# Optimization experiments

Measured on AMD Instinct MI355X. Metric: run time of the kernel, lower is better.

Reference implementation:

```python
import jax, jax.numpy as jnp
import numpy as np

N = 100000
E = 1200000
D = 64
EPS = 1e-5  # BatchNorm1d default eps


def setup_inputs() -> dict:
    key = jax.random.key(0)
    ks = jax.random.split(key, 5)
    x = jax.random.normal(ks[0], (N, D), dtype=jnp.float32)
    edge_index = jax.random.randint(ks[1], (2, E), 0, N, dtype=jnp.int32)
    W1 = jax.random.normal(ks[2], (D, D), dtype=jnp.float32) * (1.0 / np.sqrt(D))
    W2 = jax.random.normal(ks[3], (D, D), dtype=jnp.float32) * (1.0 / np.sqrt(D))
    return {
        'x': x,
        'edge_index': edge_index,
        'W1': W1,
        'b1': jnp.zeros((D,), jnp.float32),
        'gamma1': jnp.ones((D,), jnp.float32),
        'beta1': jnp.zeros((D,), jnp.float32),
        'W2': W2,
        'b2': jnp.zeros((D,), jnp.float32),
        'gamma2': jnp.ones((D,), jnp.float32),
        'beta2': jnp.zeros((D,), jnp.float32),
    }


def gcn_conv(x, src, dst, W, b):
    # GCNConv: xw = x @ W; add self-loops; symmetric deg^{-1/2} normalization;
    # scatter-add aggregation over incoming edges; + bias.
    xw = x @ W  # [N, out]
    # degree including self-loop (edge weight 1)
    deg = jnp.zeros((x.shape[0],), x.dtype).at[dst].add(1.0) + 1.0  # [N]
    dinv = jax.lax.rsqrt(deg)
    norm = dinv[src] * dinv[dst]  # [E]
    agg = jnp.zeros_like(xw).at[dst].add(norm[:, None] * xw[src])
    agg = agg + (dinv * dinv)[:, None] * xw  # self-loop term: deg^{-1} * xw
    return agg + b


def batchnorm(x, gamma, beta):
    # training-mode BatchNorm1d over node dimension (biased variance)
    mu = x.mean(axis=0)
    var = x.var(axis=0)
    return gamma * (x - mu) * jax.lax.rsqrt(var + EPS) + beta


def reference(x, edge_index, W1, b1, gamma1, beta1, W2, b2, gamma2, beta2):
    src, dst = edge_index[0], edge_index[1]
    h = gcn_conv(x, src, dst, W1, b1)
    h = jax.nn.leaky_relu(batchnorm(h, gamma1, beta1), 0.01)
    # dropout p=0.0 -> identity
    h = gcn_conv(h, src, dst, W2, b2)
    h = jax.nn.leaky_relu(batchnorm(h, gamma2, beta2), 0.01)
    return h
```

## Files before the change

kernel.cpp:

```cpp
#include <hip/hip_runtime.h>
#include <hip/hip_bf16.h>

#define NN 100000
#define NE 1200000
#define DD 64
#define EPS 1e-5f

#define NB 196
#define GEMM_BLOCKS (NN / 32)
#define HIST_BLOCKS 256
#define PART_BLOCKS 256
#define EPH ((NE + HIST_BLOCKS - 1) / HIST_BLOCKS)
#define EPB ((NE + PART_BLOCKS - 1) / PART_BLOCKS)

template <bool BN>
__device__ __forceinline__ void gemm_tile(const float* __restrict__ X,
                                          const float* __restrict__ W,
                                          __hip_bfloat16* __restrict__ XWh,
                                          const float* __restrict__ stats,
                                          const float* __restrict__ gamma,
                                          const float* __restrict__ beta,
                                          int blk) {
    __shared__ float xs[32][64];
    __shared__ float sc_s[64], sh_s[64];
    int col = threadIdx.x & 63;
    int rg  = threadIdx.x >> 6;
    int row0 = blk * 32;

    if (BN) {
        if (threadIdx.x < 64) {
            const float inv_n = 1.0f / (float)NN;
            float mu  = stats[threadIdx.x] * inv_n;
            float var = stats[64 + threadIdx.x] * inv_n - mu * mu;
            float sc  = gamma[threadIdx.x] * rsqrtf(var + EPS);
            sc_s[threadIdx.x] = sc;
            sh_s[threadIdx.x] = beta[threadIdx.x] - sc * mu;
        }
        __syncthreads();
    }

    float w[64];
#pragma unroll
    for (int k = 0; k < 64; ++k) w[k] = W[k * 64 + col];

    for (int i = threadIdx.x; i < 32 * 16; i += 256) {
        int r = i >> 4, c4 = i & 15;
        float4 v = ((const float4*)(X + (size_t)(row0 + r) * 64))[c4];
        if (BN) {
            float4 s4 = ((const float4*)sc_s)[c4];
            float4 h4 = ((const float4*)sh_s)[c4];
            v.x = s4.x * v.x + h4.x; v.x = fmaxf(v.x, 0.01f * v.x);
            v.y = s4.y * v.y + h4.y; v.y = fmaxf(v.y, 0.01f * v.y);
            v.z = s4.z * v.z + h4.z; v.z = fmaxf(v.z, 0.01f * v.z);
            v.w = s4.w * v.w + h4.w; v.w = fmaxf(v.w, 0.01f * v.w);
        }
        ((float4*)&xs[r][0])[c4] = v;
    }
    __syncthreads();

    float acc[8];
#pragma unroll
    for (int r8 = 0; r8 < 8; ++r8) {
        int r = rg * 8 + r8;
        float a = 0.0f;
#pragma unroll
        for (int k = 0; k < 64; k += 4) {
            float4 xv = *((const float4*)&xs[r][k]);
            a += xv.x * w[k] + xv.y * w[k + 1] + xv.z * w[k + 2] + xv.w * w[k + 3];
        }
        acc[r8] = a;
    }
#pragma unroll
    for (int r8 = 0; r8 < 8; ++r8)
        XWh[(size_t)(row0 + rg * 8 + r8) * 64 + col] = __float2bfloat16(acc[r8]);
}

__global__ __launch_bounds__(256) void k_l1(const float* __restrict__ X,
                                            const float* __restrict__ W,
                                            __hip_bfloat16* __restrict__ XWh,
                                            const int* __restrict__ dst,
                                            int* __restrict__ cnt196) {
    if (blockIdx.x < HIST_BLOCKS) {
        __shared__ int h[NB];
        for (int t = threadIdx.x; t < NB; t += 256) h[t] = 0;
        __syncthreads();
        int s0 = blockIdx.x * EPH;
        int s1 = s0 + EPH; if (s1 > NE) s1 = NE;
        for (int i = s0 + threadIdx.x; i < s1; i += 256)
            atomicAdd(&h[dst[i] >> 9], 1);
        __syncthreads();
        for (int t = threadIdx.x; t < NB; t += 256)
            if (h[t]) atomicAdd(&cnt196[t], h[t]);
    } else {
        gemm_tile<false>(X, W, XWh, nullptr, nullptr, nullptr,
                         (int)blockIdx.x - HIST_BLOCKS);
    }
}

__global__ __launch_bounds__(256) void k_gemm2(const float* __restrict__ X,
                                               const float* __restrict__ W,
                                               __hip_bfloat16* __restrict__ XWh,
                                               const float* __restrict__ stats,
                                               const float* __restrict__ gamma,
                                               const float* __restrict__ beta) {
    gemm_tile<true>(X, W, XWh, stats, gamma, beta, blockIdx.x);
}

__global__ __launch_bounds__(256) void k_scanb(const int* __restrict__ cnt196,
                                               int* __restrict__ bo,
                                               int* __restrict__ cur) {
    __shared__ int s[256];
    int t = threadIdx.x;
    int v = (t < NB) ? cnt196[t] : 0;
    s[t] = v;
    __syncthreads();
    for (int o = 1; o < 256; o <<= 1) {
        int u = (t >= o) ? s[t - o] : 0;
        __syncthreads();
        s[t] += u;
        __syncthreads();
    }
    if (t < NB) {
        int ex = s[t] - v;
        bo[t] = ex;
        cur[t] = ex;
    }
    if (t == 0) bo[NB] = NE;
}

__global__ __launch_bounds__(256) void k_part(const int* __restrict__ src,
                                              const int* __restrict__ dst,
                                              int* __restrict__ cur,
                                              int* __restrict__ ebuf) {
    __shared__ int h[NB];
    for (int t = threadIdx.x; t < NB; t += 256) h[t] = 0;
    __syncthreads();
    int s0 = blockIdx.x * EPB;
    int s1 = s0 + EPB; if (s1 > NE) s1 = NE;
    for (int i = s0 + threadIdx.x; i < s1; i += 256)
        atomicAdd(&h[dst[i] >> 9], 1);
    __syncthreads();
    for (int t = threadIdx.x; t < NB; t += 256) {
        int c = h[t];
        h[t] = c ? atomicAdd(&cur[t], c) : 0;
    }
    __syncthreads();
    for (int i = s0 + threadIdx.x; i < s1; i += 256) {
        int d = dst[i];
        int p = atomicAdd(&h[d >> 9], 1);
        ebuf[p] = src[i] | ((d & 511) << 17);
    }
}

__global__ __launch_bounds__(512) void k_bucket(const int* __restrict__ ebuf,
                                                const int* __restrict__ bo,
                                                int* __restrict__ off,
                                                float* __restrict__ dinv,
                                                int* __restrict__ esrc) {
    __shared__ int s[512];
    int b = blockIdx.x, t = threadIdx.x;
    int base = b << 9;
    int e0 = bo[b], e1 = bo[b + 1];
    s[t] = 0;
    __syncthreads();
    for (int e = e0 + t; e < e1; e += 512)
        atomicAdd(&s[ebuf[e] >> 17], 1);
    __syncthreads();
    int deg = s[t];
    if (base + t < NN) dinv[base + t] = rsqrtf((float)deg + 1.0f);
    for (int o = 1; o < 512; o <<= 1) {
        int u = (t >= o) ? s[t - o] : 0;
        __syncthreads();
        s[t] += u;
        __syncthreads();
    }
    int gstart = e0 + s[t] - deg;
    if (base + t < NN) off[base + t] = gstart;
    if (b == NB - 1 && t == 0) off[NN] = NE;
    __syncthreads();
    s[t] = gstart;
    __syncthreads();
    for (int e = e0 + t; e < e1; e += 512) {
        int v = ebuf[e];
        int p = atomicAdd(&s[v >> 17], 1);
        esrc[p] = v & 0x1FFFF;
    }
}

__device__ __forceinline__ void bf16x8(uint4 u, float* f) {
    f[0] = __uint_as_float(u.x << 16);
    f[1] = __uint_as_float(u.x & 0xFFFF0000u);
    f[2] = __uint_as_float(u.y << 16);
    f[3] = __uint_as_float(u.y & 0xFFFF0000u);
    f[4] = __uint_as_float(u.z << 16);
    f[5] = __uint_as_float(u.z & 0xFFFF0000u);
    f[6] = __uint_as_float(u.w << 16);
    f[7] = __uint_as_float(u.w & 0xFFFF0000u);
}

__global__ __launch_bounds__(256) void k_agg(const __hip_bfloat16* __restrict__ XWh,
                                             const int* __restrict__ off,
                                             const int* __restrict__ esrc,
                                             const float* __restrict__ dinv,
                                             float* __restrict__ out) {
    const uint4* __restrict__ XW4 = (const uint4*)XWh;
    int team = threadIdx.x >> 3;
    int sub  = threadIdx.x & 7;
    int node = blockIdx.x * 32 + team;

    float di = dinv[node];
    float a[8], b[8], r0[8], r1[8];
    uint4 us = XW4[(size_t)node * 8 + sub];
    bf16x8(us, a);
#pragma unroll
    for (int i = 0; i < 8; ++i) { a[i] *= di; b[i] = 0.0f; }

    int e0 = off[node], e1 = off[node + 1];
    int e = e0;
    for (; e + 1 < e1; e += 2) {
        int s0 = esrc[e];
        int s1 = esrc[e + 1];
        float n0 = dinv[s0], n1 = dinv[s1];
        uint4 u0 = XW4[(size_t)s0 * 8 + sub];
        uint4 u1 = XW4[(size_t)s1 * 8 + sub];
        bf16x8(u0, r0);
        bf16x8(u1, r1);
#pragma unroll
        for (int i = 0; i < 8; ++i) a[i] += n0 * r0[i];
#pragma unroll
        for (int i = 0; i < 8; ++i) b[i] += n1 * r1[i];
    }
    if (e < e1) {
        int s0 = esrc[e];
        float n0 = dinv[s0];
        uint4 u0 = XW4[(size_t)s0 * 8 + sub];
        bf16x8(u0, r0);
#pragma unroll
        for (int i = 0; i < 8; ++i) a[i] += n0 * r0[i];
    }
#pragma unroll
    for (int i = 0; i < 8; ++i) a[i] = (a[i] + b[i]) * di;

    float4* o4 = (float4*)out;
    o4[(size_t)node * 16 + sub * 2]     = make_float4(a[0], a[1], a[2], a[3]);
    o4[(size_t)node * 16 + sub * 2 + 1] = make_float4(a[4], a[5], a[6], a[7]);
}

__global__ __launch_bounds__(256) void k_stats(const float* __restrict__ X,
                                               float* __restrict__ stats, int n) {
    __shared__ float ls[4][64], lq[4][64];
    int lane = threadIdx.x & 63, rg = threadIdx.x >> 6;
    float s = 0.0f, sq = 0.0f;
    for (int r = blockIdx.x * 4 + rg; r < n; r += gridDim.x * 4) {
        float v = X[(size_t)r * 64 + lane];
        s += v; sq += v * v;
    }
    ls[rg][lane] = s; lq[rg][lane] = sq;
    __syncthreads();
    if (rg == 0) {
        s  = ls[0][lane] + ls[1][lane] + ls[2][lane] + ls[3][lane];
        sq = lq[0][lane] + lq[1][lane] + lq[2][lane] + lq[3][lane];
        atomicAdd(&stats[lane], s);
        atomicAdd(&stats[64 + lane], sq);
    }
}

__global__ __launch_bounds__(256) void k_bnact(const float* __restrict__ X,
                                               float* __restrict__ Y,
                                               const float* __restrict__ stats,
                                               const float* __restrict__ gamma,
                                               const float* __restrict__ beta,
                                               int n) {
    int lane = threadIdx.x & 63, rg = threadIdx.x >> 6;
    float inv_n = 1.0f / (float)n;
    float mu  = stats[lane] * inv_n;
    float var = stats[64 + lane] * inv_n - mu * mu;
    float sc  = gamma[lane] * rsqrtf(var + EPS);
    float sh  = beta[lane] - sc * mu;
    for (int r = blockIdx.x * 4 + rg; r < n; r += gridDim.x * 4) {
        float v = X[(size_t)r * 64 + lane];
        v = sc * v + sh;
        Y[(size_t)r * 64 + lane] = fmaxf(v, 0.01f * v);
    }
}

extern "C" void kernel_launch(void* const* d_in, const int* in_sizes, int n_in,
                              void* d_out, int out_size, void* d_ws, size_t ws_size,
                              hipStream_t stream) {
    const float* x   = (const float*)d_in[0];
    const int*   ei  = (const int*)d_in[1];
    const int*   src = ei;
    const int*   dst = ei + NE;
    const float* W1  = (const float*)d_in[2];
    const float* g1  = (const float*)d_in[4];
    const float* be1 = (const float*)d_in[5];
    const float* W2  = (const float*)d_in[6];
    const float* g2  = (const float*)d_in[8];
    const float* be2 = (const float*)d_in[9];
    float* out = (float*)d_out;

    char* ws = (char*)d_ws;
    size_t p = 0;
    auto alloc = [&](size_t bytes) {
        size_t o = p;
        p = (p + bytes + 255) & ~(size_t)255;
        return o;
    };
    int*   zeroed  = (int*)(ws + alloc(2048));
    int*   cnt196  = zeroed;
    float* stats   = (float*)(zeroed + 256);
    int*   bo      = (int*)(ws + alloc((size_t)(NB + 1) * 4));
    int*   cur     = (int*)(ws + alloc((size_t)NB * 4));
    int*   ebuf    = (int*)(ws + alloc((size_t)NE * 4));
    int*   esrc    = (int*)(ws + alloc((size_t)NE * 4));
    int*   off     = (int*)(ws + alloc((size_t)(NN + 1) * 4));
    float* dinv    = (float*)(ws + alloc((size_t)NN * 4));
    __hip_bfloat16* Ah = (__hip_bfloat16*)(ws + alloc((size_t)NN * DD * 2));
    float* B       = (float*)(ws + alloc((size_t)NN * DD * 4));
    (void)ws_size; (void)in_sizes; (void)n_in; (void)out_size;

    hipMemsetAsync(zeroed, 0, 2048, stream);

    k_l1<<<HIST_BLOCKS + GEMM_BLOCKS, 256, 0, stream>>>(x, W1, Ah, dst, cnt196);
    k_scanb<<<1, 256, 0, stream>>>(cnt196, bo, cur);
    k_part<<<PART_BLOCKS, 256, 0, stream>>>(src, dst, cur, ebuf);
    k_bucket<<<NB, 512, 0, stream>>>(ebuf, bo, off, dinv, esrc);

    k_agg<<<NN / 32, 256, 0, stream>>>(Ah, off, esrc, dinv, B);
    k_stats<<<512, 256, 0, stream>>>(B, stats, NN);

    k_gemm2<<<GEMM_BLOCKS, 256, 0, stream>>>(B, W2, Ah, stats, g1, be1);
    k_agg<<<NN / 32, 256, 0, stream>>>(Ah, off, esrc, dinv, B);
    k_stats<<<512, 256, 0, stream>>>(B, stats + 128, NN);
    k_bnact<<<1024, 256, 0, stream>>>(B, out, stats + 128, g2, be2, NN);
}
```

Before: 288.4 us.

## Co-schedule partition with first GEMM and unroll aggregation gathers by four

The histogram now runs alone, and the layer-1 GEMM tiles are merged into the partition kernel instead. This hides the heavier partition scatter behind the GEMM blocks rather than the light histogram. The aggregation loop is also unrolled from two to four edges per iteration with four independent accumulators, putting more gathers in flight. The extra accumulators and registers may lower occupancy in the aggregation kernel.

```diff
diff --git a/kernel.cpp b/kernel.cpp
--- a/kernel.cpp
+++ b/kernel.cpp
@@ -75,25 +75,71 @@
         XWh[(size_t)(row0 + rg * 8 + r8) * 64 + col] = __float2bfloat16(acc[r8]);
 }
 
-__global__ __launch_bounds__(256) void k_l1(const float* __restrict__ X,
+__global__ __launch_bounds__(256) void k_hist(const int* __restrict__ dst,
+                                              int* __restrict__ cnt196) {
+    __shared__ int h[NB];
+    for (int t = threadIdx.x; t < NB; t += 256) h[t] = 0;
+    __syncthreads();
+    int s0 = blockIdx.x * EPH;
+    int s1 = s0 + EPH; if (s1 > NE) s1 = NE;
+    for (int i = s0 + threadIdx.x; i < s1; i += 256)
+        atomicAdd(&h[dst[i] >> 9], 1);
+    __syncthreads();
+    for (int t = threadIdx.x; t < NB; t += 256)
+        if (h[t]) atomicAdd(&cnt196[t], h[t]);
+}
+
+__global__ __launch_bounds__(256) void k_scanb(const int* __restrict__ cnt196,
+                                               int* __restrict__ bo,
+                                               int* __restrict__ cur) {
+    __shared__ int s[256];
+    int t = threadIdx.x;
+    int v = (t < NB) ? cnt196[t] : 0;
+    s[t] = v;
+    __syncthreads();
+    for (int o = 1; o < 256; o <<= 1) {
+        int u = (t >= o) ? s[t - o] : 0;
+        __syncthreads();
+        s[t] += u;
+        __syncthreads();
+    }
+    if (t < NB) {
+        int ex = s[t] - v;
+        bo[t] = ex;
+        cur[t] = ex;
+    }
+    if (t == 0) bo[NB] = NE;
+}
+
+__global__ __launch_bounds__(256) void k_pg(const float* __restrict__ X,
                                             const float* __restrict__ W,
                                             __hip_bfloat16* __restrict__ XWh,
+                                            const int* __restrict__ src,
                                             const int* __restrict__ dst,
-                                            int* __restrict__ cnt196) {
-    if (blockIdx.x < HIST_BLOCKS) {
+                                            int* __restrict__ cur,
+                                            int* __restrict__ ebuf) {
+    if (blockIdx.x < PART_BLOCKS) {
         __shared__ int h[NB];
         for (int t = threadIdx.x; t < NB; t += 256) h[t] = 0;
         __syncthreads();
-        int s0 = blockIdx.x * EPH;
-        int s1 = s0 + EPH; if (s1 > NE) s1 = NE;
+        int s0 = blockIdx.x * EPB;
+        int s1 = s0 + EPB; if (s1 > NE) s1 = NE;
         for (int i = s0 + threadIdx.x; i < s1; i += 256)
             atomicAdd(&h[dst[i] >> 9], 1);
         __syncthreads();
-        for (int t = threadIdx.x; t < NB; t += 256)
-            if (h[t]) atomicAdd(&cnt196[t], h[t]);
+        for (int t = threadIdx.x; t < NB; t += 256) {
+            int c = h[t];
+            h[t] = c ? atomicAdd(&cur[t], c) : 0;
+        }
+        __syncthreads();
+        for (int i = s0 + threadIdx.x; i < s1; i += 256) {
+            int d = dst[i];
+            int p = atomicAdd(&h[d >> 9], 1);
+            ebuf[p] = src[i] | ((d & 511) << 17);
+        }
     } else {
         gemm_tile<false>(X, W, XWh, nullptr, nullptr, nullptr,
-                         (int)blockIdx.x - HIST_BLOCKS);
+                         (int)blockIdx.x - PART_BLOCKS);
     }
 }
 
@@ -104,52 +150,6 @@
                                                const float* __restrict__ gamma,
                                                const float* __restrict__ beta) {
     gemm_tile<true>(X, W, XWh, stats, gamma, beta, blockIdx.x);
-}
-
-__global__ __launch_bounds__(256) void k_scanb(const int* __restrict__ cnt196,
-                                               int* __restrict__ bo,
-                                               int* __restrict__ cur) {
-    __shared__ int s[256];
-    int t = threadIdx.x;
-    int v = (t < NB) ? cnt196[t] : 0;
-    s[t] = v;
-    __syncthreads();
-    for (int o = 1; o < 256; o <<= 1) {
-        int u = (t >= o) ? s[t - o] : 0;
-        __syncthreads();
-        s[t] += u;
-        __syncthreads();
-    }
-    if (t < NB) {
-        int ex = s[t] - v;
-        bo[t] = ex;
-        cur[t] = ex;
-    }
-    if (t == 0) bo[NB] = NE;
-}
-
-__global__ __launch_bounds__(256) void k_part(const int* __restrict__ src,
-                                              const int* __restrict__ dst,
-                                              int* __restrict__ cur,
-                                              int* __restrict__ ebuf) {
-    __shared__ int h[NB];
-    for (int t = threadIdx.x; t < NB; t += 256) h[t] = 0;
-    __syncthreads();
-    int s0 = blockIdx.x * EPB;
-    int s1 = s0 + EPB; if (s1 > NE) s1 = NE;
-    for (int i = s0 + threadIdx.x; i < s1; i += 256)
-        atomicAdd(&h[dst[i] >> 9], 1);
-    __syncthreads();
-    for (int t = threadIdx.x; t < NB; t += 256) {
-        int c = h[t];
-        h[t] = c ? atomicAdd(&cur[t], c) : 0;
-    }
-    __syncthreads();
-    for (int i = s0 + threadIdx.x; i < s1; i += 256) {
-        int d = dst[i];
-        int p = atomicAdd(&h[d >> 9], 1);
-        ebuf[p] = src[i] | ((d & 511) << 17);
-    }
 }
 
 __global__ __launch_bounds__(512) void k_bucket(const int* __restrict__ ebuf,
@@ -209,28 +209,38 @@
     int node = blockIdx.x * 32 + team;
 
     float di = dinv[node];
-    float a[8], b[8], r0[8], r1[8];
+    float a[8], b[8], c[8], d[8], r0[8], r1[8], r2[8], r3[8];
     uint4 us = XW4[(size_t)node * 8 + sub];
     bf16x8(us, a);
 #pragma unroll
-    for (int i = 0; i < 8; ++i) { a[i] *= di; b[i] = 0.0f; }
+    for (int i = 0; i < 8; ++i) { a[i] *= di; b[i] = 0.0f; c[i] = 0.0f; d[i] = 0.0f; }
 
     int e0 = off[node], e1 = off[node + 1];
     int e = e0;
-    for (; e + 1 < e1; e += 2) {
+    for (; e + 3 < e1; e += 4) {
         int s0 = esrc[e];
         int s1 = esrc[e + 1];
-        float n0 = dinv[s0], n1 = dinv[s1];
+        int s2 = esrc[e + 2];
+        int s3 = esrc[e + 3];
+        float n0 = dinv[s0], n1 = dinv[s1], n2 = dinv[s2], n3 = dinv[s3];
         uint4 u0 = XW4[(size_t)s0 * 8 + sub];
         uint4 u1 = XW4[(size_t)s1 * 8 + sub];
+        uint4 u2 = XW4[(size_t)s2 * 8 + sub];
+        uint4 u3 = XW4[(size_t)s3 * 8 + sub];
         bf16x8(u0, r0);
         bf16x8(u1, r1);
+        bf16x8(u2, r2);
+        bf16x8(u3, r3);
 #pragma unroll
         for (int i = 0; i < 8; ++i) a[i] += n0 * r0[i];
 #pragma unroll
         for (int i = 0; i < 8; ++i) b[i] += n1 * r1[i];
-    }
-    if (e < e1) {
+#pragma unroll
+        for (int i = 0; i < 8; ++i) c[i] += n2 * r2[i];
+#pragma unroll
+        for (int i = 0; i < 8; ++i) d[i] += n3 * r3[i];
+    }
+    for (; e < e1; ++e) {
         int s0 = esrc[e];
         float n0 = dinv[s0];
         uint4 u0 = XW4[(size_t)s0 * 8 + sub];
@@ -239,7 +249,7 @@
         for (int i = 0; i < 8; ++i) a[i] += n0 * r0[i];
     }
 #pragma unroll
-    for (int i = 0; i < 8; ++i) a[i] = (a[i] + b[i]) * di;
+    for (int i = 0; i < 8; ++i) a[i] = ((a[i] + b[i]) + (c[i] + d[i])) * di;
 
     float4* o4 = (float4*)out;
     o4[(size_t)node * 16 + sub * 2]     = make_float4(a[0], a[1], a[2], a[3]);
@@ -321,9 +331,9 @@
 
     hipMemsetAsync(zeroed, 0, 2048, stream);
 
-    k_l1<<<HIST_BLOCKS + GEMM_BLOCKS, 256, 0, stream>>>(x, W1, Ah, dst, cnt196);
+    k_hist<<<HIST_BLOCKS, 256, 0, stream>>>(dst, cnt196);
     k_scanb<<<1, 256, 0, stream>>>(cnt196, bo, cur);
-    k_part<<<PART_BLOCKS, 256, 0, stream>>>(src, dst, cur, ebuf);
+    k_pg<<<PART_BLOCKS + GEMM_BLOCKS, 256, 0, stream>>>(x, W1, Ah, src, dst, cur, ebuf);
     k_bucket<<<NB, 512, 0, stream>>>(ebuf, bo, off, dinv, esrc);
 
     k_agg<<<NN / 32, 256, 0, stream>>>(Ah, off, esrc, dinv, B);
```

Result: faster. 282.6 us (-2.0%).
